# Kernel optimization log

Measured on AMD Instinct MI355X. Metric: run time of the kernel, lower is better.

## Reference

```python
import jax, jax.numpy as jnp
import numpy as np
from jax import lax

DN = ('NCHW', 'OIHW', 'NCHW')

def conv2d(x, w, b, stride, pad):
    y = lax.conv_general_dilated(x, w, (stride, stride), [(pad, pad), (pad, pad)], dimension_numbers=DN)
    return y + b[None, :, None, None]

def avg_pool2(x):
    B, C, H, W = x.shape
    return x.reshape(B, C, H // 2, 2, W // 2, 2).mean(axis=(3, 5))

def lrelu(x, slope=0.01):
    return jnp.where(x >= 0, x, slope * x)

def setup_inputs() -> dict:
    key = jax.random.key(0)
    ks = jax.random.split(key, 32)
    s = 0.05
    d = {}
    d['x'] = jax.random.normal(ks[0], (32, 128, 128, 128), jnp.float32)
    d['wm'] = jax.random.normal(ks[1], (32, 32), jnp.float32)
    # WMEbeddingNet(32, 128): Linear(32,128) -> LeakyReLU(0.2) -> Linear(128,128)
    d['wm_w1'] = jax.random.normal(ks[2], (128, 32), jnp.float32) * s
    d['wm_b1'] = jnp.zeros((128,), jnp.float32)
    d['wm_w2'] = jax.random.normal(ks[3], (128, 128), jnp.float32) * s
    d['wm_b2'] = jnp.zeros((128,), jnp.float32)
    # transformation: Conv(128->64,k3,s1), Conv(64->64,k3,s2), Conv(64->64,k3,s2)
    d['tr_w1'] = jax.random.normal(ks[4], (64, 128, 3, 3), jnp.float32) * s
    d['tr_b1'] = jnp.zeros((64,), jnp.float32)
    d['tr_w2'] = jax.random.normal(ks[5], (64, 64, 3, 3), jnp.float32) * s
    d['tr_b2'] = jnp.zeros((64,), jnp.float32)
    d['tr_w3'] = jax.random.normal(ks[6], (64, 64, 3, 3), jnp.float32) * s
    d['tr_b3'] = jnp.zeros((64,), jnp.float32)
    # t1..t4: Conv(64->128,k3,s2)
    for i, k in zip((1, 2, 3, 4), (7, 8, 9, 10)):
        d[f't{i}_w'] = jax.random.normal(ks[k], (128, 64, 3, 3), jnp.float32) * s
        d[f't{i}_b'] = jnp.zeros((128,), jnp.float32)
    # Attention: Conv(64->128,k3,s2) -> GAP -> LeakyReLU -> Linear(128,4)
    d['att_cw'] = jax.random.normal(ks[11], (128, 64, 3, 3), jnp.float32) * s
    d['att_cb'] = jnp.zeros((128,), jnp.float32)
    d['att_fw'] = jax.random.normal(ks[12], (4, 128), jnp.float32) * s
    d['att_fb'] = jnp.zeros((4,), jnp.float32)
    # 4 expert kernels: (1, 4, out=64, in=128, 3, 3)
    d['expert_w'] = jax.random.normal(ks[13], (1, 4, 64, 128, 3, 3), jnp.float32)
    return d

def reference(x, wm, wm_w1, wm_b1, wm_w2, wm_b2, tr_w1, tr_b1, tr_w2, tr_b2, tr_w3, tr_b3,
              t1_w, t1_b, t2_w, t2_b, t3_w, t3_b, t4_w, t4_b, att_cw, att_cb, att_fw, att_fb, expert_w):
    B, Cin, H, W = x.shape
    # watermark embedding -> channel-wise modulation coefficients
    h = lrelu(wm @ wm_w1.T + wm_b1, 0.2)
    wm_coff = (h @ wm_w2.T + wm_b2).reshape(B, Cin, 1, 1)
    x = wm_coff * x
    # downsample then feature transformation tower
    t = avg_pool2(x)
    t = lrelu(conv2d(t, tr_w1, tr_b1, 1, 0))
    t = lrelu(conv2d(t, tr_w2, tr_b2, 2, 0))
    t = lrelu(conv2d(t, tr_w3, tr_b3, 2, 0))  # [B,64,14,14]
    # four coefficient heads (conv s2 + GAP) -> [B,4,1,128,1,1]
    def head(w, b):
        return conv2d(t, w, b, 2, 0).mean(axis=(2, 3))  # [B,128]
    agg_coff = jnp.stack([head(t1_w, t1_b), head(t2_w, t2_b), head(t3_w, t3_b), head(t4_w, t4_b)], axis=1)
    agg_coff = agg_coff.reshape(B, 4, 1, Cin, 1, 1)
    # attention over the 4 experts -> [B,4,1,1,1,1]
    a = conv2d(t, att_cw, att_cb, 2, 0).mean(axis=(2, 3))  # [B,128]
    a = lrelu(a)
    kernel_att = (a @ att_fw.T + att_fb).reshape(B, 4, 1, 1, 1, 1)
    # synthesize per-sample conv weights: [B,64,128,3,3]
    w_dyn = jnp.sum(kernel_att * (agg_coff * expert_w), axis=1)
    # per-sample grouped conv (groups = B), padding=1, stride=1
    x_r = x.reshape(1, B * Cin, H, W)
    w_r = w_dyn.reshape(B * 64, Cin, 3, 3)
    out = lax.conv_general_dilated(x_r, w_r, (1, 1), [(1, 1), (1, 1)],
                                   dimension_numbers=DN, feature_group_count=B)
    return out.reshape(B, 64, out.shape[-2], out.shape[-1])
```

## Files before the change

kernel.cpp:

```cpp
#include <hip/hip_runtime.h>
#include <hip/hip_bf16.h>
#include <cstddef>
#include <cstdint>

typedef __bf16 bf16;
typedef __attribute__((ext_vector_type(8))) __bf16 bf16x8;
typedef __attribute__((ext_vector_type(4))) __bf16 bf16x4;
typedef __attribute__((ext_vector_type(4))) float f32x4;


__global__ void k_wm_embed(const float* __restrict__ wm, const float* __restrict__ w1,
                           const float* __restrict__ b1, const float* __restrict__ w2,
                           const float* __restrict__ b2, float* __restrict__ coff) {
    int b = blockIdx.x;
    int j = threadIdx.x;
    __shared__ float h[128];
    float acc = b1[j];
    for (int k = 0; k < 32; ++k) acc += wm[b * 32 + k] * w1[j * 32 + k];
    h[j] = acc >= 0.f ? acc : 0.2f * acc;
    __syncthreads();
    float acc2 = b2[j];
    for (int k = 0; k < 128; ++k) acc2 += h[k] * w2[j * 128 + k];
    coff[b * 128 + j] = acc2;
}

__global__ __launch_bounds__(256) void k_x2nhwc_pool(
    const float* __restrict__ x, const float* __restrict__ coff,
    bf16* __restrict__ xb, bf16* __restrict__ t0b)
{
    __shared__ bf16 t[2][128 * 128];
    __shared__ float cf[128];
    const int y2 = blockIdx.x, b = blockIdx.y;
    if (threadIdx.x < 128) cf[threadIdx.x] = 0.25f * coff[b * 128 + threadIdx.x];
    const float* xp0 = x + ((size_t)b << 21) + ((size_t)(2 * y2) << 7);
    for (int i = threadIdx.x; i < 32768; i += 256) {
        int row = i >> 14, j = i & 16383;
        int c = j >> 7, xp = j & 127;
        float v = xp0[((size_t)c << 14) + (row << 7) + xp];
        t[row][(xp << 7) + (((c >> 3) ^ (xp & 15)) << 3) + (c & 7)] = (bf16)v;
    }
    __syncthreads();
    bf16* ob = xb + ((((size_t)b << 7) + 2 * y2) << 14);
    for (int j = threadIdx.x; j < 4096; j += 256) {
        int row = j >> 11, u = j & 2047;
        int xp = u >> 4, s = u & 15;
        *(bf16x8*)(ob + (row << 14) + (xp << 7) + (s << 3)) =
            *(bf16x8*)(t[row] + (xp << 7) + ((s ^ (xp & 15)) << 3));
    }
    bf16* tb = t0b + (((size_t)b * 64 + y2) << 13);
    for (int u = threadIdx.x; u < 1024; u += 256) {
        int s = u & 15, x2 = u >> 4;
        int xc0 = 2 * x2, xc1 = 2 * x2 + 1;
        bf16x8 va = *(bf16x8*)(t[0] + (xc0 << 7) + ((s ^ (xc0 & 15)) << 3));
        bf16x8 vb = *(bf16x8*)(t[0] + (xc1 << 7) + ((s ^ (xc1 & 15)) << 3));
        bf16x8 vc = *(bf16x8*)(t[1] + (xc0 << 7) + ((s ^ (xc0 & 15)) << 3));
        bf16x8 vd = *(bf16x8*)(t[1] + (xc1 << 7) + ((s ^ (xc1 & 15)) << 3));
        bf16x8 pk;
#pragma unroll
        for (int j = 0; j < 8; ++j)
            pk[j] = (bf16)(((float)va[j] + (float)vb[j] + (float)vc[j] + (float)vd[j]) * cf[s * 8 + j]);
        *(bf16x8*)(tb + (x2 << 7) + (s << 3)) = pk;
    }
}

__global__ void k_w1b(const float* __restrict__ w, bf16* __restrict__ o) {
    int i = blockIdx.x * 256 + threadIdx.x;
    if (i >= 73728) return;
    int cin = i & 127, t2 = i >> 7, co = t2 & 63, tap = t2 >> 6;
    o[i] = (bf16)(w[((size_t)co * 128 + cin) * 9 + tap]);
}

__global__ void k_w2b(const float* __restrict__ w, bf16* __restrict__ o) {
    int i = blockIdx.x * 256 + threadIdx.x;
    if (i >= 36864) return;
    int cin = i & 63, co = (i >> 6) & 63, tap = i >> 12;
    o[i] = (bf16)(w[((size_t)co * 64 + cin) * 9 + tap]);
}

template<int PAD, bool PER_BATCH_W, bool LRELU, bool HAS_BIAS, bool SWZY, bool NHWC_OUT>
__global__ __launch_bounds__(512, 4) void k_conv_mfma(
    const bf16* __restrict__ src, const bf16* __restrict__ wgt,
    const float* __restrict__ bias, void* __restrict__ outp,
    int H, int W, int Hout, int Wout)
{
    __shared__ __align__(16) bf16 xs[4 * 34 * 128];
    const int tid = threadIdx.x;
    const int wid = tid >> 6, lane = tid & 63;
    const int b = blockIdx.z;
    const int x0 = blockIdx.y << 5;
    int bx = blockIdx.x;
    const int yp = SWZY ? (((bx & 7) << 3) | (bx >> 3)) : bx;
    const int y0 = yp << 1;

    const bf16* wb = wgt + (PER_BATCH_W ? ((size_t)b * 9 * 64 * 128) : 0);
    const int qg = wid >> 1;
    const int cg = wid & 1;
    const int co0 = cg << 5;
    const int l15 = lane & 15, g = lane >> 4;
    const int q4g = (qg << 2) + g;
    const bf16* pA = wb + ((size_t)(co0 + l15) << 7) + (qg << 5) + (g << 3);
    bf16x8 A0 = *(const bf16x8*)(pA);
    bf16x8 A1 = *(const bf16x8*)(pA + (16 << 7));

    const bf16* sb = src + (((size_t)b * H) * W << 7);
    for (int k = tid; k < 4 * 34 * 16; k += 512) {
        int r = k / 544;
        int rem = k - r * 544;
        int c = rem >> 4, sp = rem & 15;
        int ys = y0 - PAD + r, xsrc = x0 - PAD + c;
        bf16x8 v = {};
        if (ys >= 0 && ys < H && xsrc >= 0 && xsrc < W)
            v = *(const bf16x8*)(sb + (((size_t)ys * W + xsrc) << 7) + ((sp ^ (c & 15)) << 3));
        *(bf16x8*)(xs + (k << 3)) = v;
    }
    __syncthreads();

    f32x4 acc[2][4] = {};
#pragma unroll
    for (int t = 0; t < 9; ++t) {
        bf16x8 A0n = A0, A1n = A1;
        if (t < 8) {
            A0n = *(const bf16x8*)(pA + ((size_t)(t + 1) << 13));
            A1n = *(const bf16x8*)(pA + ((size_t)(t + 1) << 13) + (16 << 7));
        }
        const int rt = t / 3, dx = t - 3 * rt;
        const int cb = l15 + dx;
        const int sl3 = (q4g ^ (cb & 15)) << 3;
#pragma unroll
        for (int rw = 0; rw < 2; ++rw) {
#pragma unroll
            for (int ch = 0; ch < 2; ++ch) {
                const int c0 = (ch << 4) + cb;
                bf16x8 bv = *(const bf16x8*)(xs + (((rw + rt) * 34 + c0) << 7) + sl3);
                const int n = (rw << 1) | ch;
                acc[0][n] = __builtin_amdgcn_mfma_f32_16x16x32_bf16(A0, bv, acc[0][n], 0, 0, 0);
                acc[1][n] = __builtin_amdgcn_mfma_f32_16x16x32_bf16(A1, bv, acc[1][n], 0, 0, 0);
            }
        }
        A0 = A0n; A1 = A1n;
    }

    __syncthreads();
    f32x4* redv = (f32x4*)xs;
    if (qg >= 2) {
        f32x4* wp = redv + (((cg << 1) | (qg - 2)) << 9) + lane;
#pragma unroll
        for (int m = 0; m < 2; ++m)
#pragma unroll
            for (int n = 0; n < 4; ++n)
                wp[(((m << 2) | n) << 6)] = acc[m][n];
    }
    __syncthreads();
    if (qg < 2) {
        const f32x4* rp = redv + (((cg << 1) | qg) << 9) + lane;
#pragma unroll
        for (int m = 0; m < 2; ++m)
#pragma unroll
            for (int n = 0; n < 4; ++n)
                acc[m][n] += rp[(((m << 2) | n) << 6)];
    }
    __syncthreads();
    if (qg == 1) {
        f32x4* wp = redv + (cg << 10) + lane;
#pragma unroll
        for (int m = 0; m < 2; ++m)
#pragma unroll
            for (int n = 0; n < 4; ++n)
                wp[(((m << 2) | n) << 6)] = acc[m][n];
    }
    __syncthreads();
    if (qg == 0) {
        const f32x4* rp = redv + (cg << 10) + lane;
#pragma unroll
        for (int m = 0; m < 2; ++m)
#pragma unroll
            for (int n = 0; n < 4; ++n)
                acc[m][n] += rp[(((m << 2) | n) << 6)];
#pragma unroll
        for (int m = 0; m < 2; ++m) {
#pragma unroll
            for (int n = 0; n < 4; ++n) {
                const int rw = n >> 1, ch = n & 1;
                const int xg = x0 + (ch << 4) + l15;
                const int yg = y0 + rw;
                if (xg < Wout && yg < Hout) {
                    if (NHWC_OUT) {
                        bf16x4 pk;
#pragma unroll
                        for (int reg = 0; reg < 4; ++reg) {
                            int co = co0 + m * 16 + (g << 2) + reg;
                            float v = acc[m][n][reg];
                            if (HAS_BIAS) v += bias[co];
                            if (LRELU) v = v >= 0.f ? v : 0.01f * v;
                            pk[reg] = (bf16)v;
                        }
                        *(bf16x4*)((bf16*)outp + ((((size_t)b * Hout + yg) * Wout + xg) << 6)
                                   + co0 + m * 16 + (g << 2)) = pk;
                    } else {
#pragma unroll
                        for (int reg = 0; reg < 4; ++reg) {
                            int co = co0 + m * 16 + (g << 2) + reg;
                            float v = acc[m][n][reg];
                            if (HAS_BIAS) v += bias[co];
                            if (LRELU) v = v >= 0.f ? v : 0.01f * v;
                            ((float*)outp)[(((size_t)b * 64 + co) * Hout + yg) * Wout + xg] = v;
                        }
                    }
                }
            }
        }
    }
}

__global__ __launch_bounds__(256) void k_conv_s2_mfma(
    const bf16* __restrict__ t1b, const bf16* __restrict__ w2b,
    const float* __restrict__ bias, bf16* __restrict__ t2b)
{
    __shared__ bf16 pl[2 * 3 * 33 * 64];
    const int tid = threadIdx.x;
    const int wid = tid >> 6, lane = tid & 63;
    const int y0 = blockIdx.x, b = blockIdx.y;

    for (int k = tid; k < 1536; k += 256) {
        int sl = k & 7, xsc = (k >> 3) & 63, r = k >> 9;
        if (xsc < 62) {
            int iy = 2 * y0 + r;
            bf16x8 v = *(const bf16x8*)(t1b + (((size_t)b * 3844 + iy * 62 + xsc) << 6) + (sl << 3));
            int pcol = xsc >> 1;
            int dst = (xsc & 1) * 6336 + ((r * 33 + pcol) << 6) + ((sl ^ (pcol & 7)) << 3);
            *(bf16x8*)(pl + dst) = v;
        }
    }
    __syncthreads();

    const int co0 = wid << 4;
    const int l15 = lane & 15, g = lane >> 4;
    f32x4 acc[2] = {};

    for (int r = 0; r < 3; ++r) {
#pragma unroll
        for (int dx = 0; dx < 3; ++dx) {
            const bf16* wt = w2b + ((size_t)(r * 3 + dx) << 12);
            const int pbase = (dx == 1) ? 6336 : 0;
            const int cadd = (dx == 2) ? 1 : 0;
#pragma unroll
            for (int q = 0; q < 2; ++q) {
                bf16x8 a = *(const bf16x8*)(wt + ((co0 + l15) << 6) + (q << 5) + (g << 3));
#pragma unroll
                for (int n = 0; n < 2; ++n) {
                    int col = (n << 4) + l15 + cadd;
                    int sl = ((q << 2) + g) ^ (col & 7);
                    bf16x8 bf = *(const bf16x8*)(pl + pbase + ((r * 33 + col) << 6) + (sl << 3));
                    acc[n] = __builtin_amdgcn_mfma_f32_16x16x32_bf16(a, bf, acc[n], 0, 0, 0);
                }
            }
        }
    }

#pragma unroll
    for (int n = 0; n < 2; ++n) {
        int pos = (n << 4) + l15;
        if (pos < 30) {
            bf16x4 pk;
#pragma unroll
            for (int reg = 0; reg < 4; ++reg) {
                int co = co0 + (g << 2) + reg;
                float v = acc[n][reg] + bias[co];
                v = v >= 0.f ? v : 0.01f * v;
                pk[reg] = (bf16)v;
            }
            *(bf16x4*)(t2b + ((((size_t)b * 30 + y0) * 30 + pos) << 6) + co0 + (g << 2)) = pk;
        }
    }
}

__global__ __launch_bounds__(256) void k_conv3_s2_mfma(
    const bf16* __restrict__ t2b, const bf16* __restrict__ w3b,
    const float* __restrict__ bias, float* __restrict__ t3)
{
    __shared__ bf16 pl[2 * 3 * 17 * 64];
    const int tid = threadIdx.x;
    const int wid = tid >> 6, lane = tid & 63;
    const int y0 = blockIdx.x, b = blockIdx.y;

    for (int k = tid; k < 768; k += 256) {
        int sl = k & 7, xsc = (k >> 3) & 31, r = k >> 8;
        if (xsc < 30) {
            int iy = 2 * y0 + r;
            bf16x8 v = *(const bf16x8*)(t2b + (((size_t)b * 900 + iy * 30 + xsc) << 6) + (sl << 3));
            int pcol = xsc >> 1;
            int dst = (xsc & 1) * 3264 + ((r * 17 + pcol) << 6) + ((sl ^ (pcol & 7)) << 3);
            *(bf16x8*)(pl + dst) = v;
        }
    }
    __syncthreads();

    const int co0 = wid << 4;
    const int l15 = lane & 15, g = lane >> 4;
    f32x4 acc = {};

    for (int r = 0; r < 3; ++r) {
#pragma unroll
        for (int dx = 0; dx < 3; ++dx) {
            const bf16* wt = w3b + ((size_t)(r * 3 + dx) << 12);
            const int pbase = (dx == 1) ? 3264 : 0;
            const int cadd = (dx == 2) ? 1 : 0;
#pragma unroll
            for (int q = 0; q < 2; ++q) {
                bf16x8 a = *(const bf16x8*)(wt + ((co0 + l15) << 6) + (q << 5) + (g << 3));
                int col = l15 + cadd;
                int sl = ((q << 2) + g) ^ (col & 7);
                bf16x8 bf = *(const bf16x8*)(pl + pbase + ((r * 17 + col) << 6) + (sl << 3));
                acc = __builtin_amdgcn_mfma_f32_16x16x32_bf16(a, bf, acc, 0, 0, 0);
            }
        }
    }

    if (l15 < 14) {
#pragma unroll
        for (int reg = 0; reg < 4; ++reg) {
            int co = co0 + (g << 2) + reg;
            float v = acc[reg] + bias[co];
            v = v >= 0.f ? v : 0.01f * v;
            t3[(((size_t)b * 64 + co) * 14 + y0) * 14 + l15] = v;
        }
    }
}

struct HeadPtrs { const float* w[5]; const float* b[5]; };

__global__ __launch_bounds__(256) void k_heads_fused(
    const float* __restrict__ t3, HeadPtrs hp,
    const float* __restrict__ att_fw, const float* __restrict__ att_fb,
    float* __restrict__ agg, float* __restrict__ katt)
{
    int b = blockIdx.x;
    __shared__ float S[576];
    __shared__ float ah[128];
    const float* tb = t3 + (size_t)b * 64 * 196;
    for (int i = threadIdx.x; i < 576; i += 256) {
        int ci = i / 9, k = i - ci * 9, kh = k / 3, kw = k - kh * 3;
        const float* tp = tb + ci * 196 + kh * 14 + kw;
        float s = 0.f;
#pragma unroll
        for (int oy = 0; oy < 6; ++oy)
#pragma unroll
            for (int ox = 0; ox < 6; ++ox) s += tp[oy * 28 + ox * 2];
        S[i] = s;
    }
    __syncthreads();
    for (int j = threadIdx.x; j < 640; j += 256) {
        int h = j >> 7, co = j & 127;
        const float* wp = hp.w[h] + (size_t)co * 576;
        float acc = 0.f;
        for (int k = 0; k < 576; ++k) acc += wp[k] * S[k];
        float v = acc * (1.f / 36.f) + hp.b[h][co];
        if (h < 4) agg[((size_t)b * 4 + h) * 128 + co] = v;
        else       ah[co] = v >= 0.f ? v : 0.01f * v;
    }
    __syncthreads();
    if (threadIdx.x < 4) {
        int e = threadIdx.x;
        float acc = att_fb[e];
        for (int j = 0; j < 128; ++j) acc += ah[j] * att_fw[e * 128 + j];
        katt[b * 4 + e] = acc;
    }
}

__global__ __launch_bounds__(256) void k_combine(
    const float* __restrict__ expert_w, const float* __restrict__ agg,
    const float* __restrict__ katt, const float* __restrict__ coff,
    bf16* __restrict__ wfinb)
{
    int i = blockIdx.x * 256 + threadIdx.x;
    int cin = i & 127;
    int co  = (i >> 7) & 63;
    int tap = (i >> 13) % 9;
    int b   = i / (9 << 13);
    float s = 0.f;
#pragma unroll
    for (int e = 0; e < 4; ++e)
        s += katt[b * 4 + e] * agg[((size_t)b * 4 + e) * 128 + cin]
           * expert_w[(((size_t)e * 64 + co) * 128 + cin) * 9 + tap];
    wfinb[i] = (bf16)(s * coff[b * 128 + cin]);
}

extern "C" void kernel_launch(void* const* d_in, const int* in_sizes, int n_in,
                              void* d_out, int out_size, void* d_ws, size_t ws_size,
                              hipStream_t stream) {
    const float* x      = (const float*)d_in[0];
    const float* wm     = (const float*)d_in[1];
    const float* wm_w1  = (const float*)d_in[2];
    const float* wm_b1  = (const float*)d_in[3];
    const float* wm_w2  = (const float*)d_in[4];
    const float* wm_b2  = (const float*)d_in[5];
    const float* tr_w1  = (const float*)d_in[6];
    const float* tr_b1  = (const float*)d_in[7];
    const float* tr_w2  = (const float*)d_in[8];
    const float* tr_b2  = (const float*)d_in[9];
    const float* tr_w3  = (const float*)d_in[10];
    const float* tr_b3  = (const float*)d_in[11];
    const float* t1_w   = (const float*)d_in[12];
    const float* t1_b   = (const float*)d_in[13];
    const float* t2_w   = (const float*)d_in[14];
    const float* t2_b   = (const float*)d_in[15];
    const float* t3_w   = (const float*)d_in[16];
    const float* t3_b   = (const float*)d_in[17];
    const float* t4_w   = (const float*)d_in[18];
    const float* t4_b   = (const float*)d_in[19];
    const float* att_cw = (const float*)d_in[20];
    const float* att_cb = (const float*)d_in[21];
    const float* att_fw = (const float*)d_in[22];
    const float* att_fb = (const float*)d_in[23];
    const float* expert_w = (const float*)d_in[24];
    float* out = (float*)d_out;

    float* ws = (float*)d_ws;
    float* wm_coff = ws;
    float* agg     = ws + 4096;
    float* katt    = ws + 20480;
    bf16*  w1b     = (bf16*)(ws + 20736);
    bf16*  w2b     = (bf16*)(ws + 57600);
    bf16*  w3b     = (bf16*)(ws + 76032);
    bf16*  wfinb   = (bf16*)(ws + 94464);
    bf16*  xb      = (bf16*)(ws + 1274112);
    bf16*  t0b     = (bf16*)(ws + 34828544);
    bf16*  t1b     = (bf16*)(ws + 43217152);
    bf16*  t2b     = (bf16*)(ws + 47153408);
    float* t3      = ws + 48075008;

    k_wm_embed<<<32, 128, 0, stream>>>(wm, wm_w1, wm_b1, wm_w2, wm_b2, wm_coff);

    k_x2nhwc_pool<<<dim3(64, 32), 256, 0, stream>>>(x, wm_coff, xb, t0b);

    k_w1b<<<288, 256, 0, stream>>>(tr_w1, w1b);
    k_w2b<<<144, 256, 0, stream>>>(tr_w2, w2b);
    k_w2b<<<144, 256, 0, stream>>>(tr_w3, w3b);

    k_conv_mfma<0, false, true, true, false, true><<<dim3(31, 2, 32), 512, 0, stream>>>(
        t0b, w1b, tr_b1, (void*)t1b, 64, 64, 62, 62);

    k_conv_s2_mfma<<<dim3(30, 32), 256, 0, stream>>>(t1b, w2b, tr_b2, t2b);

    k_conv3_s2_mfma<<<dim3(14, 32), 256, 0, stream>>>(t2b, w3b, tr_b3, t3);

    HeadPtrs hp;
    hp.w[0] = t1_w; hp.w[1] = t2_w; hp.w[2] = t3_w; hp.w[3] = t4_w; hp.w[4] = att_cw;
    hp.b[0] = t1_b; hp.b[1] = t2_b; hp.b[2] = t3_b; hp.b[3] = t4_b; hp.b[4] = att_cb;
    k_heads_fused<<<32, 256, 0, stream>>>(t3, hp, att_fw, att_fb, agg, katt);

    k_combine<<<9216, 256, 0, stream>>>(expert_w, agg, katt, wm_coff, wfinb);

    k_conv_mfma<1, true, false, false, true, false><<<dim3(64, 4, 32), 512, 0, stream>>>(
        xb, wfinb, nullptr, (void*)out, 128, 128, 128, 128);
}
```

Measured before the change: 476.3 us.

## Vectorize pool transpose loads, double-buffer weight prefetch, single-pass split-K reduction

```diff
diff --git a/kernel.cpp b/kernel.cpp
--- a/kernel.cpp
+++ b/kernel.cpp
@@ -7,6 +7,7 @@
 typedef __attribute__((ext_vector_type(8))) __bf16 bf16x8;
 typedef __attribute__((ext_vector_type(4))) __bf16 bf16x4;
 typedef __attribute__((ext_vector_type(4))) float f32x4;
+typedef __attribute__((ext_vector_type(2))) float f32x2;
 
 
 __global__ void k_wm_embed(const float* __restrict__ wm, const float* __restrict__ w1,
@@ -33,11 +34,18 @@
     const int y2 = blockIdx.x, b = blockIdx.y;
     if (threadIdx.x < 128) cf[threadIdx.x] = 0.25f * coff[b * 128 + threadIdx.x];
     const float* xp0 = x + ((size_t)b << 21) + ((size_t)(2 * y2) << 7);
-    for (int i = threadIdx.x; i < 32768; i += 256) {
-        int row = i >> 14, j = i & 16383;
-        int c = j >> 7, xp = j & 127;
-        float v = xp0[((size_t)c << 14) + (row << 7) + xp];
-        t[row][(xp << 7) + (((c >> 3) ^ (xp & 15)) << 3) + (c & 7)] = (bf16)v;
+    for (int i = threadIdx.x; i < 2048; i += 256) {
+        int xp2 = (i & 63) << 1, slot = (i >> 6) & 15, row = i >> 10;
+        const float* src = xp0 + ((size_t)(slot * 8) << 14) + (row << 7) + xp2;
+        bf16x8 pk0, pk1;
+#pragma unroll
+        for (int j = 0; j < 8; ++j) {
+            f32x2 v = *(const f32x2*)(src + ((size_t)j << 14));
+            pk0[j] = (bf16)v[0];
+            pk1[j] = (bf16)v[1];
+        }
+        *(bf16x8*)(t[row] + (xp2 << 7) + ((slot ^ (xp2 & 15)) << 3)) = pk0;
+        *(bf16x8*)(t[row] + ((xp2 + 1) << 7) + ((slot ^ ((xp2 + 1) & 15)) << 3)) = pk1;
     }
     __syncthreads();
     bf16* ob = xb + ((((size_t)b << 7) + 2 * y2) << 14);
@@ -83,7 +91,8 @@
     const float* __restrict__ bias, void* __restrict__ outp,
     int H, int W, int Hout, int Wout)
 {
-    __shared__ __align__(16) bf16 xs[4 * 34 * 128];
+    __shared__ __align__(16) unsigned char smem[49152];
+    bf16* xs = (bf16*)smem;
     const int tid = threadIdx.x;
     const int wid = tid >> 6, lane = tid & 63;
     const int b = blockIdx.z;
@@ -99,8 +108,10 @@
     const int l15 = lane & 15, g = lane >> 4;
     const int q4g = (qg << 2) + g;
     const bf16* pA = wb + ((size_t)(co0 + l15) << 7) + (qg << 5) + (g << 3);
-    bf16x8 A0 = *(const bf16x8*)(pA);
-    bf16x8 A1 = *(const bf16x8*)(pA + (16 << 7));
+    bf16x8 Pa0 = *(const bf16x8*)(pA);
+    bf16x8 Pa1 = *(const bf16x8*)(pA + (16 << 7));
+    bf16x8 Pb0 = *(const bf16x8*)(pA + ((size_t)1 << 13));
+    bf16x8 Pb1 = *(const bf16x8*)(pA + ((size_t)1 << 13) + (16 << 7));
 
     const bf16* sb = src + (((size_t)b * H) * W << 7);
     for (int k = tid; k < 4 * 34 * 16; k += 512) {
@@ -118,11 +129,8 @@
     f32x4 acc[2][4] = {};
 #pragma unroll
     for (int t = 0; t < 9; ++t) {
-        bf16x8 A0n = A0, A1n = A1;
-        if (t < 8) {
-            A0n = *(const bf16x8*)(pA + ((size_t)(t + 1) << 13));
-            A1n = *(const bf16x8*)(pA + ((size_t)(t + 1) << 13) + (16 << 7));
-        }
+        const bf16x8 A0 = (t & 1) ? Pb0 : Pa0;
+        const bf16x8 A1 = (t & 1) ? Pb1 : Pa1;
         const int rt = t / 3, dx = t - 3 * rt;
         const int cb = l15 + dx;
         const int sl3 = (q4g ^ (cb & 15)) << 3;
@@ -137,13 +145,17 @@
                 acc[1][n] = __builtin_amdgcn_mfma_f32_16x16x32_bf16(A1, bv, acc[1][n], 0, 0, 0);
             }
         }
-        A0 = A0n; A1 = A1n;
-    }
-
-    __syncthreads();
-    f32x4* redv = (f32x4*)xs;
-    if (qg >= 2) {
-        f32x4* wp = redv + (((cg << 1) | (qg - 2)) << 9) + lane;
+        if (t + 2 < 9) {
+            bf16x8 n0 = *(const bf16x8*)(pA + ((size_t)(t + 2) << 13));
+            bf16x8 n1 = *(const bf16x8*)(pA + ((size_t)(t + 2) << 13) + (16 << 7));
+            if (t & 1) { Pb0 = n0; Pb1 = n1; } else { Pa0 = n0; Pa1 = n1; }
+        }
+    }
+
+    __syncthreads();
+    f32x4* redv = (f32x4*)smem;
+    if (qg > 0) {
+        f32x4* wp = redv + ((((qg - 1) << 1) | cg) << 9) + lane;
 #pragma unroll
         for (int m = 0; m < 2; ++m)
 #pragma unroll
@@ -151,31 +163,16 @@
                 wp[(((m << 2) | n) << 6)] = acc[m][n];
     }
     __syncthreads();
-    if (qg < 2) {
-        const f32x4* rp = redv + (((cg << 1) | qg) << 9) + lane;
-#pragma unroll
-        for (int m = 0; m < 2; ++m)
-#pragma unroll
-            for (int n = 0; n < 4; ++n)
-                acc[m][n] += rp[(((m << 2) | n) << 6)];
-    }
-    __syncthreads();
-    if (qg == 1) {
-        f32x4* wp = redv + (cg << 10) + lane;
-#pragma unroll
-        for (int m = 0; m < 2; ++m)
-#pragma unroll
-            for (int n = 0; n < 4; ++n)
-                wp[(((m << 2) | n) << 6)] = acc[m][n];
-    }
-    __syncthreads();
     if (qg == 0) {
-        const f32x4* rp = redv + (cg << 10) + lane;
-#pragma unroll
-        for (int m = 0; m < 2; ++m)
-#pragma unroll
-            for (int n = 0; n < 4; ++n)
-                acc[m][n] += rp[(((m << 2) | n) << 6)];
+#pragma unroll
+        for (int s = 0; s < 3; ++s) {
+            const f32x4* rp = redv + (((s << 1) | cg) << 9) + lane;
+#pragma unroll
+            for (int m = 0; m < 2; ++m)
+#pragma unroll
+                for (int n = 0; n < 4; ++n)
+                    acc[m][n] += rp[(((m << 2) | n) << 6)];
+        }
 #pragma unroll
         for (int m = 0; m < 2; ++m) {
 #pragma unroll
```

After: 465.8 us. 2.2% less time.
